# Kernel optimization log

Measured on AMD Instinct MI355X. Metric: run time of the kernel, lower is better.

Reference implementation:

```python
import jax, jax.numpy as jnp
import numpy as np

N_NODES = 50000
N_EDGES = 400000
LATENT = 128
HIDDEN = 512
N_HEADS = 2          # latent // 64, NodeAttn default num_heads
HEAD_DIM = LATENT // N_HEADS
N_GRAPHS = 500
LN_EPS = 1e-5


def setup_inputs() -> dict:
    key = jax.random.key(0)
    ks = jax.random.split(key, 24)
    s = 0.02
    inp = {
        "edges": jax.random.randint(ks[0], (2, N_EDGES), 0, N_NODES, dtype=jnp.int32),
        "node_feat": jax.random.normal(ks[1], (N_NODES, LATENT), jnp.float32),
        "edge_attr": jax.random.normal(ks[2], (N_EDGES, LATENT), jnp.float32),
        "u": jax.random.normal(ks[3], (N_GRAPHS, LATENT), jnp.float32),
        "num_nodes": jnp.full((N_GRAPHS,), N_NODES // N_GRAPHS, jnp.int32),
        # NodeAttn params (shared for sent/received calls, as in the module)
        "w1": jax.random.normal(ks[4], (3 * LATENT, LATENT), jnp.float32) * s,
        "b1": jnp.zeros((LATENT,), jnp.float32),
        "w2": jax.random.normal(ks[5], (N_HEADS, HEAD_DIM), jnp.float32) * s,
        "w3": jax.random.normal(ks[6], (2 * LATENT, LATENT), jnp.float32) * s,
        "b3": jnp.zeros((LATENT,), jnp.float32),
        # Encoder MLP: 4*latent -> hidden -> hidden -> latent, LN before ReLU
        "mw0": jax.random.normal(ks[7], (4 * LATENT, HIDDEN), jnp.float32) * s,
        "mb0": jnp.zeros((HIDDEN,), jnp.float32),
        "ls0": jnp.ones((HIDDEN,), jnp.float32),
        "lb0": jnp.zeros((HIDDEN,), jnp.float32),
        "mw1": jax.random.normal(ks[8], (HIDDEN, HIDDEN), jnp.float32) * s,
        "mb1": jnp.zeros((HIDDEN,), jnp.float32),
        "ls1": jnp.ones((HIDDEN,), jnp.float32),
        "lb1": jnp.zeros((HIDDEN,), jnp.float32),
        "mw2": jax.random.normal(ks[9], (HIDDEN, LATENT), jnp.float32) * s,
        "mb2": jnp.zeros((LATENT,), jnp.float32),
    }
    return inp


def _layer_norm(x, scale, bias):
    mu = jnp.mean(x, axis=-1, keepdims=True)
    var = jnp.mean(jnp.square(x - mu), axis=-1, keepdims=True)
    return (x - mu) * jax.lax.rsqrt(var + LN_EPS) * scale + bias


def _node_attn(q, k, ea, index, n_nodes, w1, b1, w2, w3, b3):
    # per-edge multi-head scores -> segment softmax over destination index -> scatter-add
    h = jax.nn.leaky_relu(jnp.concatenate([q, k, ea], axis=-1) @ w1 + b1, 0.2)
    h = h.reshape(-1, N_HEADS, HEAD_DIM)                    # [E, H, D]
    logits = jnp.einsum("ehd,hd->eh", h, w2)                 # [E, H]
    m = jax.ops.segment_max(logits, index, num_segments=n_nodes)
    m = jnp.where(jnp.isfinite(m), m, 0.0)                   # empty segments
    e = jnp.exp(logits - m[index])
    z = jax.ops.segment_sum(e, index, num_segments=n_nodes)
    alpha = e / (z[index] + 1e-16)                           # [E, H]
    v = (jnp.concatenate([k, ea], axis=-1) @ w3 + b3).reshape(-1, N_HEADS, HEAD_DIM)
    out = jax.ops.segment_sum(alpha[..., None] * v, index, num_segments=n_nodes)
    return out.reshape(n_nodes, LATENT)


def reference(edges, node_feat, edge_attr, u, num_nodes, w1, b1, w2, w3, b3,
              mw0, mb0, ls0, lb0, mw1, mb1, ls1, lb1, mw2, mb2):
    n = node_feat.shape[0]
    row, col = edges[0], edges[1]
    sent = _node_attn(node_feat[row], node_feat[col], edge_attr, row, n, w1, b1, w2, w3, b3)
    recv = _node_attn(node_feat[col], node_feat[row], edge_attr, col, n, w1, b1, w2, w3, b3)
    glob = jnp.repeat(u, num_nodes, axis=0, total_repeat_length=n)
    x = jnp.concatenate([node_feat, sent, recv, glob], axis=1)   # [N, 4*latent]
    h = jax.nn.relu(_layer_norm(x @ mw0 + mb0, ls0, lb0))
    h = jax.nn.relu(_layer_norm(h @ mw1 + mb1, ls1, lb1))
    return h @ mw2 + mb2
```

## Files before the change

### kernel.cpp

```cpp
#include <hip/hip_runtime.h>
#include <math.h>

#define LATENT 128

typedef __attribute__((ext_vector_type(8))) short bf16x8;
typedef __attribute__((ext_vector_type(4))) float f32x4;
typedef __attribute__((ext_vector_type(2))) float f32x2;
typedef __attribute__((ext_vector_type(2))) int i32x2;
typedef __attribute__((ext_vector_type(2))) unsigned u32x2;

union U4B { uint4 u; bf16x8 v; };

template <typename T>
__device__ __forceinline__ T ntl(const T* p) { return __builtin_nontemporal_load(p); }

__device__ __forceinline__ unsigned short f2bf(float f) {
    unsigned int x = __float_as_uint(f);
    unsigned int r = (x + 0x7fffu + ((x >> 16) & 1u)) >> 16;
    return (unsigned short)r;
}
__device__ __forceinline__ float bf2f(unsigned short h) {
    return __uint_as_float(((unsigned int)h) << 16);
}
__device__ __forceinline__ unsigned pk2(float a, float b) {
    return (unsigned)f2bf(a) | ((unsigned)f2bf(b) << 16);
}

__device__ __forceinline__ void gld16(const void* g, void* l) {
    __builtin_amdgcn_global_load_lds(
        (const __attribute__((address_space(1))) unsigned int*)g,
        (__attribute__((address_space(3))) unsigned int*)l, 16, 0, 0);
}

__global__ void k_gid(const int* __restrict__ num_nodes, int G, int n, int* __restrict__ gid) {
    __shared__ int goff[1025];
    if (threadIdx.x == 0) {
        int acc = 0;
        for (int g = 0; g < G; ++g) { goff[g] = acc; acc += num_nodes[g]; }
        goff[G] = acc;
    }
    __syncthreads();
    for (int g = 0; g < G; ++g) {
        int s = goff[g];
        int e = goff[g + 1]; if (e > n) e = n;
        for (int i = s + (int)threadIdx.x; i < e; i += blockDim.x) gid[i] = g;
    }
}

#define FN  1152
#define FE3 1248
#define FEV 1280
__global__ __launch_bounds__(256) void k_pack2(const float* __restrict__ mw0,
                                               const float* __restrict__ mw1,
                                               const float* __restrict__ mw2,
                                               const float* __restrict__ w1,
                                               const float* __restrict__ w3,
                                               uint4* __restrict__ pw) {
    int tid = blockIdx.x * 256 + threadIdx.x;
    if (tid >= 1312 * 64) return;
    int fid = tid >> 6, lane = tid & 63;
    const float* src; int kt, nt, N;
    if (fid < 512)       { src = mw0;            kt = fid >> 5;           nt = fid & 31;           N = 512; }
    else if (fid < 1024) { src = mw1;            kt = (fid - 512) >> 5;   nt = (fid - 512) & 31;   N = 512; }
    else if (fid < 1152) { src = mw2;            kt = (fid - 1024) >> 3;  nt = (fid - 1024) & 7;   N = 128; }
    else if (fid < 1184) { src = w1;             kt = (fid - 1152) >> 3;  nt = (fid - 1152) & 7;   N = 128; }
    else if (fid < 1216) { src = w1 + 128 * 128; kt = (fid - 1184) >> 3;  nt = (fid - 1184) & 7;   N = 128; }
    else if (fid < 1248) { src = w3;             kt = (fid - 1216) >> 3;  nt = (fid - 1216) & 7;   N = 128; }
    else if (fid < 1280) { src = w1 + 256 * 128; kt = (fid - 1248) >> 3;  nt = (fid - 1248) & 7;   N = 128; }
    else                 { src = w3 + 128 * 128; kt = (fid - 1280) >> 3;  nt = (fid - 1280) & 7;   N = 128; }
    int col = nt * 16 + (lane & 15);
    int k0 = kt * 32 + (lane >> 4) * 8;
    unsigned int w[4];
#pragma unroll
    for (int p = 0; p < 4; ++p) {
        unsigned int lo = f2bf(src[(size_t)(k0 + 2 * p) * N + col]);
        unsigned int hi = f2bf(src[(size_t)(k0 + 2 * p + 1) * N + col]);
        w[p] = lo | (hi << 16);
    }
    pw[(size_t)fid * 64 + lane] = make_uint4(w[0], w[1], w[2], w[3]);
}

__global__ void k_count(const int* __restrict__ edges, int E,
                        int* __restrict__ deg_s, int* __restrict__ deg_r) {
    int e = blockIdx.x * 256 + threadIdx.x;
    if (e < E) { atomicAdd(&deg_s[edges[e]], 1); atomicAdd(&deg_r[edges[E + e]], 1); }
}

__global__ __launch_bounds__(1024) void k_scan(const int* __restrict__ deg, int n,
                                               int* __restrict__ rowptr, int* __restrict__ cursor) {
    __shared__ int wsum[16];
    int t = threadIdx.x;
    int chunk = (n + 1023) / 1024;
    int s = t * chunk; if (s > n) s = n;
    int epos = s + chunk; if (epos > n) epos = n;
    int sum = 0;
    for (int i = s; i < epos; ++i) sum += deg[i];
    int lane = t & 63, wid = t >> 6;
    int v = sum;
#pragma unroll
    for (int d = 1; d < 64; d <<= 1) { int o = __shfl_up(v, d); if (lane >= d) v += o; }
    if (lane == 63) wsum[wid] = v;
    __syncthreads();
    if (t < 16) {
        int wv = wsum[t];
#pragma unroll
        for (int d = 1; d < 16; d <<= 1) { int o = __shfl_up(wv, d, 16); if (t >= d) wv += o; }
        wsum[t] = wv;
    }
    __syncthreads();
    int woff = wid ? wsum[wid - 1] : 0;
    int run = v + woff - sum;
    for (int i = s; i < epos; ++i) { rowptr[i] = run; cursor[i] = run; run += deg[i]; }
    if (t == 1023) rowptr[n] = run;
}

__global__ void k_fill(const int* __restrict__ edges, int E,
                       int* __restrict__ cur_s, int* __restrict__ cur_r,
                       int2* __restrict__ eo_s, int2* __restrict__ eo_r,
                       int* __restrict__ sm_s, int* __restrict__ sm_r) {
    int e = blockIdx.x * 256 + threadIdx.x;
    if (e < E) {
        int r = edges[e], c = edges[E + e];
        int p = atomicAdd(&cur_s[r], 1); eo_s[p] = make_int2(e, c); sm_s[e] = p;
        int q = atomicAdd(&cur_r[c], 1); eo_r[q] = make_int2(e, r); sm_r[e] = q;
    }
}

__global__ __launch_bounds__(512) void k_nodepre2(const float* __restrict__ nf, int n,
                                                  const uint4* __restrict__ pw,
                                                  unsigned short* __restrict__ PQK,
                                                  unsigned short* __restrict__ PVh) {
    __shared__ uint4 xs[32 * 64];
    int t = threadIdx.x, lane = t & 63, w = t >> 6;
    int wr = w >> 2, wc = w & 3, l15 = lane & 15, lg = lane >> 4;
    int base = blockIdx.x * 128;
#pragma unroll
    for (int it = 0; it < 4; ++it) {
        int chunk = t + it * 512;
        int row = chunk >> 4, k8 = chunk & 15, k = k8 * 8;
        int node = base + row;
        f32x4 v0 = (f32x4)(0.f), v1 = (f32x4)(0.f);
        if (node < n) {
            const f32x4* s4 = (const f32x4*)(nf + (size_t)node * 128 + k);
            v0 = ntl(s4); v1 = ntl(s4 + 1);
        }
        uint4 pkv;
        pkv.x = pk2(v0.x, v0.y); pkv.y = pk2(v0.z, v0.w);
        pkv.z = pk2(v1.x, v1.y); pkv.w = pk2(v1.z, v1.w);
        int kt = k >> 5, g = (k >> 3) & 3;
        xs[(kt * 8 + (row >> 4)) * 64 + g * 16 + (row & 15)] = pkv;
    }
    __syncthreads();
    f32x4 acc[4][6];
#pragma unroll
    for (int rt = 0; rt < 4; ++rt)
#pragma unroll
        for (int ct = 0; ct < 6; ++ct) acc[rt][ct] = (f32x4)(0.f);
    for (int kt = 0; kt < 4; ++kt) {
        U4B a[4];
#pragma unroll
        for (int rt = 0; rt < 4; ++rt) a[rt].u = xs[(kt * 8 + wr * 4 + rt) * 64 + lane];
        U4B b[6];
#pragma unroll
        for (int ct = 0; ct < 6; ++ct) {
            int nt = wc * 6 + ct;
            int mat = nt >> 3, ntm = nt & 7;
            b[ct].u = pw[(size_t)(FN + mat * 32 + kt * 8 + ntm) * 64 + lane];
        }
#pragma unroll
        for (int rt = 0; rt < 4; ++rt)
#pragma unroll
            for (int ct = 0; ct < 6; ++ct)
                acc[rt][ct] = __builtin_amdgcn_mfma_f32_16x16x32_bf16(a[rt].v, b[ct].v, acc[rt][ct], 0, 0, 0);
    }
#pragma unroll
    for (int rt = 0; rt < 4; ++rt)
#pragma unroll
        for (int ct = 0; ct < 6; ++ct) {
            int nt = wc * 6 + ct;
#pragma unroll
            for (int reg = 0; reg < 4; ++reg) {
                int node = base + (wr * 4 + rt) * 16 + lg * 4 + reg;
                if (node < n) {
                    unsigned short hv = f2bf(acc[rt][ct][reg]);
                    if (nt < 16) PQK[(size_t)node * 256 + nt * 16 + l15] = hv;
                    else         PVh[(size_t)node * 128 + (nt - 16) * 16 + l15] = hv;
                }
            }
        }
}

__global__ __launch_bounds__(256) void k_eproj1(const int* __restrict__ edges,
                                                const float* __restrict__ ea, int E,
                                                const uint4* __restrict__ pw,
                                                const unsigned short* __restrict__ PQK,
                                                const float* __restrict__ b1,
                                                const float* __restrict__ w2,
                                                const int* __restrict__ sm_s,
                                                const int* __restrict__ sm_r,
                                                unsigned short* __restrict__ EVg,
                                                float* __restrict__ ess2, float* __restrict__ ers2) {
    __shared__ uint4 xs[16 * 64];
    __shared__ unsigned short edata[64 * 128];
    int t = threadIdx.x, lane = t & 63, w = t >> 6;
    int wc = w, l15 = lane & 15, lg = lane >> 4;
    int base = blockIdx.x * 64;
#pragma unroll
    for (int it = 0; it < 4; ++it) {
        int chunk = t + it * 256;
        int row = chunk >> 4, k8 = chunk & 15, k = k8 * 8;
        int e = base + row;
        f32x4 v0 = (f32x4)(0.f), v1 = (f32x4)(0.f);
        if (e < E) {
            const f32x4* s4 = (const f32x4*)(ea + (size_t)e * 128 + k);
            v0 = ntl(s4); v1 = ntl(s4 + 1);
        }
        uint4 pkv;
        pkv.x = pk2(v0.x, v0.y); pkv.y = pk2(v0.z, v0.w);
        pkv.z = pk2(v1.x, v1.y); pkv.w = pk2(v1.z, v1.w);
        int kt = k >> 5, g = (k >> 3) & 3;
        xs[(kt * 4 + (row >> 4)) * 64 + g * 16 + (row & 15)] = pkv;
    }
    __syncthreads();
    f32x4 acc[4][4];
#pragma unroll
    for (int rt = 0; rt < 4; ++rt)
#pragma unroll
        for (int ct = 0; ct < 4; ++ct) acc[rt][ct] = (f32x4)(0.f);
    for (int kt = 0; kt < 4; ++kt) {
        U4B a[4];
#pragma unroll
        for (int rt = 0; rt < 4; ++rt) a[rt].u = xs[(kt * 4 + rt) * 64 + lane];
        U4B b[4];
        b[0].u = pw[(size_t)(FE3 + kt * 8 + wc * 2 + 0) * 64 + lane];
        b[1].u = pw[(size_t)(FE3 + kt * 8 + wc * 2 + 1) * 64 + lane];
        b[2].u = pw[(size_t)(FEV + kt * 8 + wc * 2 + 0) * 64 + lane];
        b[3].u = pw[(size_t)(FEV + kt * 8 + wc * 2 + 1) * 64 + lane];
#pragma unroll
        for (int rt = 0; rt < 4; ++rt)
#pragma unroll
            for (int ct = 0; ct < 4; ++ct)
                acc[rt][ct] = __builtin_amdgcn_mfma_f32_16x16x32_bf16(a[rt].v, b[ct].v, acc[rt][ct], 0, 0, 0);
    }
#pragma unroll
    for (int rt = 0; rt < 4; ++rt)
#pragma unroll
        for (int cc = 0; cc < 2; ++cc) {
            int col = (wc * 2 + cc) * 16 + l15;
#pragma unroll
            for (int reg = 0; reg < 4; ++reg) {
                int e_loc = rt * 16 + lg * 4 + reg;
                int e = base + e_loc;
                if (e < E) __builtin_nontemporal_store(f2bf(acc[rt][2 + cc][reg]),
                                                       &EVg[(size_t)e * 128 + col]);
                edata[e_loc * 128 + col] = f2bf(acc[rt][cc][reg]);
            }
        }
    __syncthreads();
    int esub = lane >> 3, dg = lane & 7;
    float b1r[16], w2r[16];
    {
        const float4* b4 = (const float4*)(b1 + dg * 16);
        const float4* w4 = (const float4*)(w2 + (dg >> 2) * 64 + (dg & 3) * 16);
#pragma unroll
        for (int q = 0; q < 4; ++q) {
            float4 bv = b4[q], wv = w4[q];
            b1r[q * 4 + 0] = bv.x; b1r[q * 4 + 1] = bv.y; b1r[q * 4 + 2] = bv.z; b1r[q * 4 + 3] = bv.w;
            w2r[q * 4 + 0] = wv.x; w2r[q * 4 + 1] = wv.y; w2r[q * 4 + 2] = wv.z; w2r[q * 4 + 3] = wv.w;
        }
    }
#pragma unroll
    for (int it = 0; it < 2; ++it) {
        int e_loc = w * 16 + it * 8 + esub;
        int e = base + e_loc;
        if (e >= E) break;
        int r = edges[e], c = edges[E + e];
        const uint4* Aqr = (const uint4*)(PQK + ((size_t)r << 8) + dg * 16);
        const uint4* Akc = (const uint4*)(PQK + ((size_t)c << 8) + 128 + dg * 16);
        const uint4* Aqc = (const uint4*)(PQK + ((size_t)c << 8) + dg * 16);
        const uint4* Akr = (const uint4*)(PQK + ((size_t)r << 8) + 128 + dg * 16);
        const uint4* Ae3 = (const uint4*)(&edata[e_loc * 128 + dg * 16]);
        float ps = 0.f, pr = 0.f;
#pragma unroll
        for (int half = 0; half < 2; ++half) {
            uint4 uqr = Aqr[half], ukc = Akc[half], uqc = Aqc[half], ukr = Akr[half], ue3 = Ae3[half];
            unsigned wqr[4] = {uqr.x, uqr.y, uqr.z, uqr.w};
            unsigned wkc[4] = {ukc.x, ukc.y, ukc.z, ukc.w};
            unsigned wqc[4] = {uqc.x, uqc.y, uqc.z, uqc.w};
            unsigned wkr[4] = {ukr.x, ukr.y, ukr.z, ukr.w};
            unsigned we3[4] = {ue3.x, ue3.y, ue3.z, ue3.w};
#pragma unroll
            for (int q = 0; q < 4; ++q) {
#pragma unroll
                for (int hl = 0; hl < 2; ++hl) {
                    int i = half * 8 + q * 2 + hl;
                    float fqr = hl ? __uint_as_float(wqr[q] & 0xffff0000u) : __uint_as_float(wqr[q] << 16);
                    float fkc = hl ? __uint_as_float(wkc[q] & 0xffff0000u) : __uint_as_float(wkc[q] << 16);
                    float fqc = hl ? __uint_as_float(wqc[q] & 0xffff0000u) : __uint_as_float(wqc[q] << 16);
                    float fkr = hl ? __uint_as_float(wkr[q] & 0xffff0000u) : __uint_as_float(wkr[q] << 16);
                    float fe3 = hl ? __uint_as_float(we3[q] & 0xffff0000u) : __uint_as_float(we3[q] << 16);
                    float com = fe3 + b1r[i];
                    float hs = fqr + fkc + com; hs = hs > 0.f ? hs : 0.2f * hs;
                    float hr = fqc + fkr + com; hr = hr > 0.f ? hr : 0.2f * hr;
                    ps += hs * w2r[i]; pr += hr * w2r[i];
                }
            }
        }
        ps += __shfl_xor(ps, 1); ps += __shfl_xor(ps, 2);
        pr += __shfl_xor(pr, 1); pr += __shfl_xor(pr, 2);
        float Es = expf(ps), Er = expf(pr);
        if (dg == 0) {
            __builtin_nontemporal_store(Es, &ess2[(size_t)sm_s[e] * 2]);
            __builtin_nontemporal_store(Er, &ers2[(size_t)sm_r[e] * 2]);
        } else if (dg == 4) {
            __builtin_nontemporal_store(Es, &ess2[(size_t)sm_s[e] * 2 + 1]);
            __builtin_nontemporal_store(Er, &ers2[(size_t)sm_r[e] * 2 + 1]);
        }
    }
}

__global__ __launch_bounds__(256) void k_aggr(int E, int n,
                                              const int* __restrict__ rps, const int2* __restrict__ eo_s,
                                              const int* __restrict__ rpr, const int2* __restrict__ eo_r,
                                              const float* __restrict__ ess2, const float* __restrict__ ers2,
                                              const unsigned short* __restrict__ PVh,
                                              const unsigned short* __restrict__ EVg,
                                              const float* __restrict__ b3,
                                              unsigned short* __restrict__ out_sh,
                                              unsigned short* __restrict__ out_rh) {
    int w = threadIdx.x >> 6, lane = threadIdx.x & 63;
    int unit = blockIdx.x * 4 + w;
    if (unit >= 2 * n) return;
    bool sent = unit < n;
    int node = sent ? unit : unit - n;
    const int*   rp = sent ? rps : rpr;
    const i32x2* eo = (const i32x2*)(sent ? eo_s : eo_r);
    const float* ex = sent ? ess2 : ers2;
    int s0 = rp[node], s1 = rp[node + 1];
    float b3a = b3[2 * lane], b3b = b3[2 * lane + 1];
    const unsigned* EV32 = (const unsigned*)EVg;
    const unsigned* PV32 = (const unsigned*)PVh;
    float z0 = 0.f, z1 = 0.f, acca = 0.f, accb = 0.f;
    int j = s0;
    for (; j + 4 <= s1; j += 4) {
        i32x2 p[4]; f32x2 ez[4]; unsigned ev[4], pv[4];
#pragma unroll
        for (int q = 0; q < 4; ++q) p[q] = ntl(eo + j + q);
#pragma unroll
        for (int q = 0; q < 4; ++q) ez[q] = ntl((const f32x2*)(ex + 2 * (j + q)));
#pragma unroll
        for (int q = 0; q < 4; ++q) ev[q] = ntl(EV32 + (size_t)p[q].x * 64 + lane);
#pragma unroll
        for (int q = 0; q < 4; ++q) pv[q] = PV32[(size_t)p[q].y * 64 + lane];
#pragma unroll
        for (int q = 0; q < 4; ++q) {
            float va = __uint_as_float(ev[q] << 16) + __uint_as_float(pv[q] << 16) + b3a;
            float vb = __uint_as_float(ev[q] & 0xffff0000u) + __uint_as_float(pv[q] & 0xffff0000u) + b3b;
            z0 += ez[q].x; z1 += ez[q].y;
            float aw = (lane < 32) ? ez[q].x : ez[q].y;
            acca += aw * va; accb += aw * vb;
        }
    }
    for (; j < s1; ++j) {
        i32x2 p = ntl(eo + j);
        f32x2 ez = ntl((const f32x2*)(ex + 2 * j));
        unsigned ev = ntl(EV32 + (size_t)p.x * 64 + lane);
        unsigned pv = PV32[(size_t)p.y * 64 + lane];
        float va = __uint_as_float(ev << 16) + __uint_as_float(pv << 16) + b3a;
        float vb = __uint_as_float(ev & 0xffff0000u) + __uint_as_float(pv & 0xffff0000u) + b3b;
        z0 += ez.x; z1 += ez.y;
        float aw = (lane < 32) ? ez.x : ez.y;
        acca += aw * va; accb += aw * vb;
    }
    float zz = (lane < 32) ? z0 : z1;
    float rz = 1.f / (zz + 1e-16f);
    unsigned o = pk2(acca * rz, accb * rz);
    unsigned* outp = (unsigned*)(sent ? out_sh : out_rh);
    outp[(size_t)node * 64 + lane] = o;
}

__global__ __launch_bounds__(512) void k_mlp9(
    const float* __restrict__ nf, const unsigned short* __restrict__ out_sh,
    const unsigned short* __restrict__ out_rh,
    const float* __restrict__ u, const int* __restrict__ gid, int n,
    const uint4* __restrict__ pw,
    const float* __restrict__ mb0, const float* __restrict__ ls0, const float* __restrict__ lb0,
    const float* __restrict__ mb1, const float* __restrict__ ls1, const float* __restrict__ lb1,
    const float* __restrict__ mb2, float* __restrict__ out) {
    extern __shared__ char smem[];
    char* hx = smem;
    char* bb = smem + 65536;
    float2* red = (float2*)(smem + 131072);

    int t = threadIdx.x, lane = t & 63, w = t >> 6;
    int wr = w >> 2, wc = w & 3, l15 = lane & 15, lg = lane >> 4;
    int base = blockIdx.x * 64;

    auto stage32 = [&](int fragbase, int d) {
        const uint4* src = pw + (size_t)fragbase * 64;
        char* dst = bb + (size_t)d * 32768;
#pragma unroll
        for (int q = 0; q < 4; ++q)
            gld16(src + q * 512 + t, dst + ((size_t)q * 512 + t) * 16);
    };
    auto stage8 = [&](int fragbase, int d) {
        const uint4* src = pw + (size_t)fragbase * 64;
        char* dst = bb + (size_t)d * 32768;
        gld16(src + t, dst + (size_t)t * 16);
    };

    stage32(0, 0);
#pragma unroll
    for (int it = 0; it < 16; ++it) {
        int chunk = t + it * 512;
        int row = chunk >> 7, kq = chunk & 127;
        int k = kq * 4;
        int node = base + row;
        u32x2 p = (u32x2)(0u);
        if (node < n) {
            int kk = k & 127;
            if (k < 128) {
                f32x4 v = ntl((const f32x4*)(nf + (size_t)node * 128 + kk));
                p.x = pk2(v.x, v.y); p.y = pk2(v.z, v.w);
            } else if (k < 384) {
                const unsigned short* s = (k < 256 ? out_sh : out_rh) + (size_t)node * 128 + kk;
                p = ntl((const u32x2*)s);
            } else {
                f32x4 v = *(const f32x4*)(u + (size_t)gid[node] * 128 + kk);
                p.x = pk2(v.x, v.y); p.y = pk2(v.z, v.w);
            }
        }
        int addr = (row * 1024 + k * 2) ^ ((row & 7) << 4);
        *(u32x2*)(hx + addr) = p;
    }
    __syncthreads();

    f32x4 acc[2][8];
    int buf = 0;
#pragma unroll
    for (int layer = 0; layer < 2; ++layer) {
        const float* MB = layer ? mb1 : mb0;
        const float* LS = layer ? ls1 : ls0;
        const float* LB = layer ? lb1 : lb0;
        const int fbase = layer ? 512 : 0;
#pragma unroll
        for (int rt = 0; rt < 2; ++rt)
#pragma unroll
            for (int ct = 0; ct < 8; ++ct) acc[rt][ct] = (f32x4)(0.f);

        for (int kt = 0; kt < 16; ++kt) {
            if (kt < 15)            stage32(fbase + (kt + 1) * 32, buf ^ 1);
            else if (layer == 0)    stage32(512, buf ^ 1);
            else                    stage8(1024, buf ^ 1);
            U4B b[8];
#pragma unroll
            for (int ct = 0; ct < 8; ++ct)
                b[ct].u = *(const uint4*)(bb + (size_t)buf * 32768 + ((wc * 8 + ct) * 64 + lane) * 16);
            U4B a[2];
#pragma unroll
            for (int rt = 0; rt < 2; ++rt) {
                int row = wr * 32 + rt * 16 + l15;
                int addr = (row * 1024 + kt * 64 + lg * 16) ^ ((row & 7) << 4);
                a[rt].u = *(const uint4*)(hx + addr);
            }
            __builtin_amdgcn_s_setprio(1);
#pragma unroll
            for (int rt = 0; rt < 2; ++rt)
#pragma unroll
                for (int ct = 0; ct < 8; ++ct)
                    acc[rt][ct] = __builtin_amdgcn_mfma_f32_16x16x32_bf16(a[rt].v, b[ct].v, acc[rt][ct], 0, 0, 0);
            __builtin_amdgcn_s_setprio(0);
            __syncthreads();
            buf ^= 1;
        }

        float mbv[8], lsv[8], lbv[8];
#pragma unroll
        for (int ct = 0; ct < 8; ++ct) {
            int col = wc * 128 + ct * 16 + l15;
            mbv[ct] = MB[col]; lsv[ct] = LS[col]; lbv[ct] = LB[col];
        }
#pragma unroll
        for (int rt = 0; rt < 2; ++rt)
#pragma unroll
            for (int reg = 0; reg < 4; ++reg) {
                float p = 0.f, q = 0.f;
#pragma unroll
                for (int ct = 0; ct < 8; ++ct) {
                    float y = acc[rt][ct][reg] + mbv[ct];
                    acc[rt][ct][reg] = y;
                    p += y; q += y * y;
                }
#pragma unroll
                for (int d = 1; d < 16; d <<= 1) { p += __shfl_xor(p, d); q += __shfl_xor(q, d); }
                if (l15 == 0) {
                    int row = wr * 32 + rt * 16 + lg * 4 + reg;
                    red[row * 4 + wc] = make_float2(p, q);
                }
            }
        __syncthreads();
#pragma unroll
        for (int rt = 0; rt < 2; ++rt)
#pragma unroll
            for (int reg = 0; reg < 4; ++reg) {
                int row = wr * 32 + rt * 16 + lg * 4 + reg;
                float2 r0 = red[row * 4 + 0], r1 = red[row * 4 + 1];
                float2 r2 = red[row * 4 + 2], r3 = red[row * 4 + 3];
                float S = r0.x + r1.x + r2.x + r3.x;
                float S2 = r0.y + r1.y + r2.y + r3.y;
                float mu = S * (1.f / 512.f);
                float var = S2 * (1.f / 512.f) - mu * mu;
                float rs = rsqrtf(var + 1e-5f);
                int rswz = (row & 7) << 4;
#pragma unroll
                for (int ct = 0; ct < 8; ++ct) {
                    float h = (acc[rt][ct][reg] - mu) * rs * lsv[ct] + lbv[ct];
                    h = fmaxf(h, 0.f);
                    int col = wc * 128 + ct * 16 + l15;
                    int addr = (row * 1024 + col * 2) ^ rswz;
                    *(unsigned short*)(hx + addr) = f2bf(h);
                }
            }
        __syncthreads();
    }

    f32x4 a2[2][2];
#pragma unroll
    for (int rt = 0; rt < 2; ++rt)
#pragma unroll
        for (int ct = 0; ct < 2; ++ct) a2[rt][ct] = (f32x4)(0.f);
    for (int kt = 0; kt < 16; ++kt) {
        if (kt < 15) stage8(1024 + (kt + 1) * 8, buf ^ 1);
        U4B b[2];
#pragma unroll
        for (int ct = 0; ct < 2; ++ct)
            b[ct].u = *(const uint4*)(bb + (size_t)buf * 32768 + ((wc * 2 + ct) * 64 + lane) * 16);
        U4B a[2];
#pragma unroll
        for (int rt = 0; rt < 2; ++rt) {
            int row = wr * 32 + rt * 16 + l15;
            int addr = (row * 1024 + kt * 64 + lg * 16) ^ ((row & 7) << 4);
            a[rt].u = *(const uint4*)(hx + addr);
        }
        __builtin_amdgcn_s_setprio(1);
#pragma unroll
        for (int rt = 0; rt < 2; ++rt)
#pragma unroll
            for (int ct = 0; ct < 2; ++ct)
                a2[rt][ct] = __builtin_amdgcn_mfma_f32_16x16x32_bf16(a[rt].v, b[ct].v, a2[rt][ct], 0, 0, 0);
        __builtin_amdgcn_s_setprio(0);
        __syncthreads();
        buf ^= 1;
    }
    float mb2v[2];
#pragma unroll
    for (int ct = 0; ct < 2; ++ct) mb2v[ct] = mb2[wc * 32 + ct * 16 + l15];
#pragma unroll
    for (int rt = 0; rt < 2; ++rt)
#pragma unroll
        for (int reg = 0; reg < 4; ++reg) {
            int node = base + wr * 32 + rt * 16 + lg * 4 + reg;
            if (node < n) {
#pragma unroll
                for (int ct = 0; ct < 2; ++ct)
                    __builtin_nontemporal_store(a2[rt][ct][reg] + mb2v[ct],
                        &out[(size_t)node * 128 + wc * 32 + ct * 16 + l15]);
            }
        }
}

extern "C" void kernel_launch(void* const* d_in, const int* in_sizes, int n_in,
                              void* d_out, int out_size, void* d_ws, size_t ws_size,
                              hipStream_t stream) {
    const int*   edges     = (const int*)d_in[0];
    const float* nf        = (const float*)d_in[1];
    const float* ea        = (const float*)d_in[2];
    const float* u         = (const float*)d_in[3];
    const int*   num_nodes = (const int*)d_in[4];
    const float* w1  = (const float*)d_in[5];
    const float* b1  = (const float*)d_in[6];
    const float* w2  = (const float*)d_in[7];
    const float* w3  = (const float*)d_in[8];
    const float* b3  = (const float*)d_in[9];
    const float* mw0 = (const float*)d_in[10];
    const float* mb0 = (const float*)d_in[11];
    const float* ls0 = (const float*)d_in[12];
    const float* lb0 = (const float*)d_in[13];
    const float* mw1 = (const float*)d_in[14];
    const float* mb1 = (const float*)d_in[15];
    const float* ls1 = (const float*)d_in[16];
    const float* lb1 = (const float*)d_in[17];
    const float* mw2 = (const float*)d_in[18];
    const float* mb2 = (const float*)d_in[19];

    int E = in_sizes[0] / 2;
    int n = in_sizes[1] / LATENT;
    int G = in_sizes[4];
    float* out = (float*)d_out;

    char* wsb = (char*)d_ws;
    size_t off = 0;
    auto alloc = [&](size_t bytes) { void* p = (void*)(wsb + off); off += (bytes + 15) & ~(size_t)15; return p; };
    uint4*          pw     = (uint4*)alloc((size_t)1312 * 64 * 16);
    unsigned short* PQK    = (unsigned short*)alloc((size_t)n * 256 * 2);
    unsigned short* PVh    = (unsigned short*)alloc((size_t)n * 128 * 2);
    unsigned short* EVg    = (unsigned short*)alloc((size_t)E * 128 * 2);
    float*          ess2   = (float*)alloc((size_t)E * 2 * 4);
    float*          ers2   = (float*)alloc((size_t)E * 2 * 4);
    unsigned short* out_sh = (unsigned short*)alloc((size_t)n * 128 * 2);
    unsigned short* out_rh = (unsigned short*)alloc((size_t)n * 128 * 2);
    int*            gid    = (int*)alloc((size_t)n * 4);
    int*            deg_s  = (int*)alloc((size_t)n * 4);
    int*            deg_r  = (int*)alloc((size_t)n * 4);
    int*            cur_s  = (int*)alloc((size_t)n * 4);
    int*            cur_r  = (int*)alloc((size_t)n * 4);
    int*            rps    = (int*)alloc((size_t)(n + 1) * 4);
    int*            rpr    = (int*)alloc((size_t)(n + 1) * 4);
    int2*           eo_s   = (int2*)alloc((size_t)E * 8);
    int2*           eo_r   = (int2*)alloc((size_t)E * 8);
    int*            sm_s   = (int*)alloc((size_t)E * 4);
    int*            sm_r   = (int*)alloc((size_t)E * 4);

    hipMemsetAsync(deg_s, 0, (size_t)2 * n * 4 + 16, stream);

    hipFuncSetAttribute((const void*)k_mlp9, hipFuncAttributeMaxDynamicSharedMemorySize, 133120);

    k_gid<<<1, 256, 0, stream>>>(num_nodes, G, n, gid);
    k_pack2<<<(1312 * 64 + 255) / 256, 256, 0, stream>>>(mw0, mw1, mw2, w1, w3, pw);
    k_count<<<(E + 255) / 256, 256, 0, stream>>>(edges, E, deg_s, deg_r);
    k_scan<<<1, 1024, 0, stream>>>(deg_s, n, rps, cur_s);
    k_scan<<<1, 1024, 0, stream>>>(deg_r, n, rpr, cur_r);
    k_fill<<<(E + 255) / 256, 256, 0, stream>>>(edges, E, cur_s, cur_r, eo_s, eo_r, sm_s, sm_r);
    k_nodepre2<<<(n + 127) / 128, 512, 0, stream>>>(nf, n, pw, PQK, PVh);
    k_eproj1<<<(E + 63) / 64, 256, 0, stream>>>(edges, ea, E, pw, PQK, b1, w2, sm_s, sm_r,
                                                EVg, ess2, ers2);
    k_aggr<<<(2 * n + 3) / 4, 256, 0, stream>>>(E, n, rps, eo_s, rpr, eo_r,
                                                ess2, ers2, PVh, EVg, b3, out_sh, out_rh);
    k_mlp9<<<(n + 63) / 64, 512, 133120, stream>>>(nf, out_sh, out_rh, u, gid, n, pw,
                                                   mb0, ls0, lb0, mb1, ls1, lb1, mb2, out);
}
```

Before: 859.6 us.

## Scatter edge value projections into CSR order for contiguous aggregation reads

The edge-value projection EV is now written twice, once in sent-CSR order and once in received-CSR order, using the slot maps sm_s/sm_r. The aggregation kernel then reads EV sequentially by CSR position instead of gathering it by edge id. This also lets the CSR entries shrink from (edge, other) pairs to just the other-node index. In exchange, k_eproj1 writes twice the EV bytes through scattered 256-byte stores and stages them in an extra shared buffer, and the workspace grows by E*256 bytes.

```diff
diff --git a/kernel.cpp b/kernel.cpp
--- a/kernel.cpp
+++ b/kernel.cpp
@@ -8,6 +8,7 @@
 typedef __attribute__((ext_vector_type(2))) float f32x2;
 typedef __attribute__((ext_vector_type(2))) int i32x2;
 typedef __attribute__((ext_vector_type(2))) unsigned u32x2;
+typedef __attribute__((ext_vector_type(4))) unsigned u32x4;
 
 union U4B { uint4 u; bf16x8 v; };
 
@@ -116,13 +117,13 @@
 
 __global__ void k_fill(const int* __restrict__ edges, int E,
                        int* __restrict__ cur_s, int* __restrict__ cur_r,
-                       int2* __restrict__ eo_s, int2* __restrict__ eo_r,
+                       int* __restrict__ os_s, int* __restrict__ os_r,
                        int* __restrict__ sm_s, int* __restrict__ sm_r) {
     int e = blockIdx.x * 256 + threadIdx.x;
     if (e < E) {
         int r = edges[e], c = edges[E + e];
-        int p = atomicAdd(&cur_s[r], 1); eo_s[p] = make_int2(e, c); sm_s[e] = p;
-        int q = atomicAdd(&cur_r[c], 1); eo_r[q] = make_int2(e, r); sm_r[e] = q;
+        int p = atomicAdd(&cur_s[r], 1); os_s[p] = c; sm_s[e] = p;
+        int q = atomicAdd(&cur_r[c], 1); os_r[q] = r; sm_r[e] = q;
     }
 }
 
@@ -198,10 +199,12 @@
                                                 const float* __restrict__ w2,
                                                 const int* __restrict__ sm_s,
                                                 const int* __restrict__ sm_r,
-                                                unsigned short* __restrict__ EVg,
+                                                unsigned short* __restrict__ EVs,
+                                                unsigned short* __restrict__ EVr,
                                                 float* __restrict__ ess2, float* __restrict__ ers2) {
     __shared__ uint4 xs[16 * 64];
     __shared__ unsigned short edata[64 * 128];
+    __shared__ unsigned short evdata[64 * 128];
     int t = threadIdx.x, lane = t & 63, w = t >> 6;
     int wc = w, l15 = lane & 15, lg = lane >> 4;
     int base = blockIdx.x * 64;
@@ -250,13 +253,24 @@
 #pragma unroll
             for (int reg = 0; reg < 4; ++reg) {
                 int e_loc = rt * 16 + lg * 4 + reg;
-                int e = base + e_loc;
-                if (e < E) __builtin_nontemporal_store(f2bf(acc[rt][2 + cc][reg]),
-                                                       &EVg[(size_t)e * 128 + col]);
-                edata[e_loc * 128 + col] = f2bf(acc[rt][cc][reg]);
+                edata[e_loc * 128 + col]  = f2bf(acc[rt][cc][reg]);
+                evdata[e_loc * 128 + col] = f2bf(acc[rt][2 + cc][reg]);
             }
         }
     __syncthreads();
+    {
+        int e4 = lane >> 4, piece = lane & 15;
+#pragma unroll
+        for (int i = 0; i < 4; ++i) {
+            int e_loc = w * 16 + i * 4 + e4;
+            int e = base + e_loc;
+            if (e < E) {
+                u32x4 v = *(const u32x4*)&evdata[e_loc * 128 + piece * 8];
+                __builtin_nontemporal_store(v, (u32x4*)(EVs + (size_t)sm_s[e] * 128 + piece * 8));
+                __builtin_nontemporal_store(v, (u32x4*)(EVr + (size_t)sm_r[e] * 128 + piece * 8));
+            }
+        }
+    }
     int esub = lane >> 3, dg = lane & 7;
     float b1r[16], w2r[16];
     {
@@ -319,12 +333,13 @@
     }
 }
 
-__global__ __launch_bounds__(256) void k_aggr(int E, int n,
-                                              const int* __restrict__ rps, const int2* __restrict__ eo_s,
-                                              const int* __restrict__ rpr, const int2* __restrict__ eo_r,
+__global__ __launch_bounds__(256) void k_aggr(int n,
+                                              const int* __restrict__ rps, const int* __restrict__ os_s,
+                                              const int* __restrict__ rpr, const int* __restrict__ os_r,
                                               const float* __restrict__ ess2, const float* __restrict__ ers2,
                                               const unsigned short* __restrict__ PVh,
-                                              const unsigned short* __restrict__ EVg,
+                                              const unsigned short* __restrict__ EVs,
+                                              const unsigned short* __restrict__ EVr,
                                               const float* __restrict__ b3,
                                               unsigned short* __restrict__ out_sh,
                                               unsigned short* __restrict__ out_rh) {
@@ -334,24 +349,24 @@
     bool sent = unit < n;
     int node = sent ? unit : unit - n;
     const int*   rp = sent ? rps : rpr;
-    const i32x2* eo = (const i32x2*)(sent ? eo_s : eo_r);
+    const int*   os = sent ? os_s : os_r;
     const float* ex = sent ? ess2 : ers2;
+    const unsigned* EVx = (const unsigned*)(sent ? EVs : EVr);
+    const unsigned* PV32 = (const unsigned*)PVh;
     int s0 = rp[node], s1 = rp[node + 1];
     float b3a = b3[2 * lane], b3b = b3[2 * lane + 1];
-    const unsigned* EV32 = (const unsigned*)EVg;
-    const unsigned* PV32 = (const unsigned*)PVh;
     float z0 = 0.f, z1 = 0.f, acca = 0.f, accb = 0.f;
     int j = s0;
     for (; j + 4 <= s1; j += 4) {
-        i32x2 p[4]; f32x2 ez[4]; unsigned ev[4], pv[4];
-#pragma unroll
-        for (int q = 0; q < 4; ++q) p[q] = ntl(eo + j + q);
+        int oth[4]; f32x2 ez[4]; unsigned ev[4], pv[4];
+#pragma unroll
+        for (int q = 0; q < 4; ++q) oth[q] = os[j + q];
 #pragma unroll
         for (int q = 0; q < 4; ++q) ez[q] = ntl((const f32x2*)(ex + 2 * (j + q)));
 #pragma unroll
-        for (int q = 0; q < 4; ++q) ev[q] = ntl(EV32 + (size_t)p[q].x * 64 + lane);
-#pragma unroll
-        for (int q = 0; q < 4; ++q) pv[q] = PV32[(size_t)p[q].y * 64 + lane];
+        for (int q = 0; q < 4; ++q) ev[q] = ntl(EVx + (size_t)(j + q) * 64 + lane);
+#pragma unroll
+        for (int q = 0; q < 4; ++q) pv[q] = PV32[(size_t)oth[q] * 64 + lane];
 #pragma unroll
         for (int q = 0; q < 4; ++q) {
             float va = __uint_as_float(ev[q] << 16) + __uint_as_float(pv[q] << 16) + b3a;
@@ -362,10 +377,10 @@
         }
     }
     for (; j < s1; ++j) {
-        i32x2 p = ntl(eo + j);
+        int oth = os[j];
         f32x2 ez = ntl((const f32x2*)(ex + 2 * j));
-        unsigned ev = ntl(EV32 + (size_t)p.x * 64 + lane);
-        unsigned pv = PV32[(size_t)p.y * 64 + lane];
+        unsigned ev = ntl(EVx + (size_t)j * 64 + lane);
+        unsigned pv = PV32[(size_t)oth * 64 + lane];
         float va = __uint_as_float(ev << 16) + __uint_as_float(pv << 16) + b3a;
         float vb = __uint_as_float(ev & 0xffff0000u) + __uint_as_float(pv & 0xffff0000u) + b3b;
         z0 += ez.x; z1 += ez.y;
@@ -604,7 +619,8 @@
     uint4*          pw     = (uint4*)alloc((size_t)1312 * 64 * 16);
     unsigned short* PQK    = (unsigned short*)alloc((size_t)n * 256 * 2);
     unsigned short* PVh    = (unsigned short*)alloc((size_t)n * 128 * 2);
-    unsigned short* EVg    = (unsigned short*)alloc((size_t)E * 128 * 2);
+    unsigned short* EVs    = (unsigned short*)alloc((size_t)E * 128 * 2);
+    unsigned short* EVr    = (unsigned short*)alloc((size_t)E * 128 * 2);
     float*          ess2   = (float*)alloc((size_t)E * 2 * 4);
     float*          ers2   = (float*)alloc((size_t)E * 2 * 4);
     unsigned short* out_sh = (unsigned short*)alloc((size_t)n * 128 * 2);
@@ -616,8 +632,8 @@
     int*            cur_r  = (int*)alloc((size_t)n * 4);
     int*            rps    = (int*)alloc((size_t)(n + 1) * 4);
     int*            rpr    = (int*)alloc((size_t)(n + 1) * 4);
-    int2*           eo_s   = (int2*)alloc((size_t)E * 8);
-    int2*           eo_r   = (int2*)alloc((size_t)E * 8);
+    int*            os_s   = (int*)alloc((size_t)E * 4);
+    int*            os_r   = (int*)alloc((size_t)E * 4);
     int*            sm_s   = (int*)alloc((size_t)E * 4);
     int*            sm_r   = (int*)alloc((size_t)E * 4);
 
@@ -630,12 +646,12 @@
     k_count<<<(E + 255) / 256, 256, 0, stream>>>(edges, E, deg_s, deg_r);
     k_scan<<<1, 1024, 0, stream>>>(deg_s, n, rps, cur_s);
     k_scan<<<1, 1024, 0, stream>>>(deg_r, n, rpr, cur_r);
-    k_fill<<<(E + 255) / 256, 256, 0, stream>>>(edges, E, cur_s, cur_r, eo_s, eo_r, sm_s, sm_r);
+    k_fill<<<(E + 255) / 256, 256, 0, stream>>>(edges, E, cur_s, cur_r, os_s, os_r, sm_s, sm_r);
     k_nodepre2<<<(n + 127) / 128, 512, 0, stream>>>(nf, n, pw, PQK, PVh);
     k_eproj1<<<(E + 63) / 64, 256, 0, stream>>>(edges, ea, E, pw, PQK, b1, w2, sm_s, sm_r,
-                                                EVg, ess2, ers2);
-    k_aggr<<<(2 * n + 3) / 4, 256, 0, stream>>>(E, n, rps, eo_s, rpr, eo_r,
-                                                ess2, ers2, PVh, EVg, b3, out_sh, out_rh);
+                                                EVs, EVr, ess2, ers2);
+    k_aggr<<<(2 * n + 3) / 4, 256, 0, stream>>>(n, rps, os_s, rpr, os_r,
+                                                ess2, ers2, PVh, EVs, EVr, b3, out_sh, out_rh);
     k_mlp9<<<(n + 63) / 64, 512, 133120, stream>>>(nf, out_sh, out_rh, u, gid, n, pw,
                                                    mb0, ls0, lb0, mb1, ls1, lb1, mb2, out);
 }
```

After: 842.8 us. No clear change (-2.0%).
